# Kernel optimization log

Measured on AMD Instinct MI355X. Metric: run time of the kernel, lower is better.

Reference implementation:

```python
import jax, jax.numpy as jnp
import numpy as np

EMBED = 512
HEADS = 8
HEAD_DIM = EMBED // HEADS


def setup_inputs() -> dict:
    key = jax.random.key(0)
    ks = jax.random.split(key, 9)
    N, L = 4, 2048
    values = jax.random.normal(ks[0], (N, L, EMBED), dtype=jnp.float32)
    keys = jax.random.normal(ks[1], (N, L, EMBED), dtype=jnp.float32)
    query = jax.random.normal(ks[2], (N, L, EMBED), dtype=jnp.float32)
    mask = jax.random.randint(ks[3], (N, 1, 1, L), 0, 2, dtype=jnp.int32)
    s_h = 1.0 / np.sqrt(HEAD_DIM).astype(np.float32)
    s_e = 1.0 / np.sqrt(EMBED).astype(np.float32)
    Wv = jax.random.normal(ks[4], (HEAD_DIM, HEAD_DIM), dtype=jnp.float32) * s_h
    Wk = jax.random.normal(ks[5], (HEAD_DIM, HEAD_DIM), dtype=jnp.float32) * s_h
    Wq = jax.random.normal(ks[6], (HEAD_DIM, HEAD_DIM), dtype=jnp.float32) * s_h
    Wo = jax.random.normal(ks[7], (EMBED, EMBED), dtype=jnp.float32) * s_e
    bo = jnp.zeros((EMBED,), dtype=jnp.float32)
    return {"values": values, "keys": keys, "query": query, "mask": mask,
            "Wv": Wv, "Wk": Wk, "Wq": Wq, "Wo": Wo, "bo": bo}


def reference(values, keys, query, mask, Wv, Wk, Wq, Wo, bo):
    N, Lq, E = query.shape
    D = Wv.shape[0]
    H = E // D
    Lk = keys.shape[1]
    # split heads: [N, L, H, D]
    v = values.reshape(N, values.shape[1], H, D)
    k = keys.reshape(N, Lk, H, D)
    q = query.reshape(N, Lq, H, D)
    # per-head linear projections (nn.Linear: x @ W^T, no bias)
    v = jnp.einsum("nlhd,ed->nlhe", v, Wv)
    k = jnp.einsum("nlhd,ed->nlhe", k, Wk)
    q = jnp.einsum("nlhd,ed->nlhe", q, Wq)
    # energy: [N, H, Lq, Lk]
    energy = jnp.einsum("nqhd,nkhd->nhqk", q, k)
    energy = jnp.where(mask == 0, jnp.float32(-1e20), energy)
    # NOTE: original scales by sqrt(embed_size), not sqrt(head_dim)
    attn = jax.nn.softmax(energy / jnp.sqrt(jnp.float32(E)), axis=3)
    out = jnp.einsum("nhqk,nkhd->nqhd", attn, v).reshape(N, Lq, E)
    return out @ Wo.T + bo
```

## Files before the change

### kernel.cpp

```cpp
#include <hip/hip_runtime.h>

#define LSEQ 2048
#define EMB  512
#define NH   8
#define HD   64
#define NBATCH 4
#define QSCALE (0.044194173824159216f * 1.4426950408889634f)

using short8  = __attribute__((ext_vector_type(8))) short;
using short4v = __attribute__((ext_vector_type(4))) short;
using f32x4   = __attribute__((ext_vector_type(4))) float;

__device__ __forceinline__ short bf16r(float f) {
  union { float f; unsigned u; } x; x.f = f;
  unsigned r = x.u + 0x7FFFu + ((x.u >> 16) & 1u);
  return (short)(r >> 16);
}

__device__ __forceinline__ float exp2v(float x) {
  float r;
  asm("v_exp_f32 %0, %1" : "=v"(r) : "v"(x));
  return r;
}

__device__ __forceinline__ unsigned cvtpk(float lo, float hi) {
  unsigned r;
  asm("v_cvt_pk_bf16_f32 %0, %1, %2" : "=v"(r) : "v"(lo), "v"(hi));
  return r;
}

__device__ __forceinline__ void stage16(const void* g, void* l) {
  __builtin_amdgcn_global_load_lds(
      (const __attribute__((address_space(1))) unsigned int*)g,
      (__attribute__((address_space(3))) unsigned int*)l, 16, 0, 0);
}

__device__ __forceinline__ short8 cvt8(const float* __restrict__ p) {
  float4 a = ((const float4*)p)[0];
  float4 b = ((const float4*)p)[1];
  short8 r;
  r[0]=bf16r(a.x); r[1]=bf16r(a.y); r[2]=bf16r(a.z); r[3]=bf16r(a.w);
  r[4]=bf16r(b.x); r[5]=bf16r(b.y); r[6]=bf16r(b.z); r[7]=bf16r(b.w);
  return r;
}

__device__ __forceinline__ short8 ld8(const short* __restrict__ p) {
  return *(const short8*)p;
}

__global__ __launch_bounds__(256) void prep_kernel(
    const int* __restrict__ mask, float* __restrict__ fbias,
    int* __restrict__ kidx, int* __restrict__ meta,
    const float* __restrict__ Wq, const float* __restrict__ Wk,
    const float* __restrict__ Wv, short* __restrict__ Wqb,
    short* __restrict__ Wkb, short* __restrict__ Wvb) {
  __shared__ int ssum[256];
  int b = blockIdx.x;
  int tid = threadIdx.x;
  if (b < 4) {
    int n = b;
    int base = n * LSEQ;
    int loc[8], c = 0;
#pragma unroll
    for (int j = 0; j < 8; j++) { loc[j] = mask[base + tid * 8 + j] != 0; c += loc[j]; }
    ssum[tid] = c;
    __syncthreads();
    for (int off = 1; off < 256; off <<= 1) {
      int v = (tid >= off) ? ssum[tid - off] : 0;
      __syncthreads();
      ssum[tid] += v;
      __syncthreads();
    }
    int total = ssum[255];
    int excl = ssum[tid] - c;
    int qz = (total == 0);
#pragma unroll
    for (int j = 0; j < 8; j++) {
      int i = tid * 8 + j;
      kidx[base + i] = qz ? i : 0;
      fbias[base + i] = (qz || i < total) ? 0.f : -1e30f;
    }
    __syncthreads();
    if (!qz) {
      int pos = excl;
#pragma unroll
      for (int j = 0; j < 8; j++)
        if (loc[j]) { kidx[base + pos] = tid * 8 + j; pos++; }
    }
    if (tid == 0) {
      meta[n] = qz ? (LSEQ / 64) : ((total + 63) >> 6);
      meta[4 + n] = qz;
    }
  } else {
    int t = (b - 4) >> 2;
    int i = ((b - 4) & 3) * 256 + tid;
    const float* W = (t == 0) ? Wq : (t == 1) ? Wk : Wv;
    short* O = (t == 0) ? Wqb : (t == 1) ? Wkb : Wvb;
    float sc = (t == 0) ? QSCALE : 1.f;
    float4 v = ((const float4*)W)[i];
    short4v r;
    r[0]=bf16r(v.x*sc); r[1]=bf16r(v.y*sc); r[2]=bf16r(v.z*sc); r[3]=bf16r(v.w*sc);
    ((short4v*)O)[i] = r;
  }
}

__global__ __launch_bounds__(256) void proj_kernel(
    const float* __restrict__ keys, const float* __restrict__ values,
    const short* __restrict__ Wkb, const short* __restrict__ Wvb,
    const int* __restrict__ kidx, const int* __restrict__ meta,
    short* __restrict__ Kp, short* __restrict__ Vt) {
  __shared__ short tile[64][72];
  int t = blockIdx.y + 1;
  const float* x = (t == 1) ? keys : values;
  const short* W = (t == 1) ? Wkb  : Wvb;
  int idx = blockIdx.x;
  int lt = idx & 31, h = (idx >> 5) & 7, n = idx >> 8;
  int tid = threadIdx.x, lane = tid & 63, w = tid >> 6;
  int row16 = lane & 15, g = lane >> 4;
  int lbase = lt * 64 + w * 16;

  if (lbase >= ((meta[n] + 1) & ~1) * 64) return;
  int gidx = kidx[n * LSEQ + lbase + row16];
  const float* xr = x + ((size_t)(n * LSEQ + gidx)) * EMB + h * HD + g * 8;
  short8 a0 = cvt8(xr);
  short8 a1 = cvt8(xr + 32);

  f32x4 acc[4];
#pragma unroll
  for (int et = 0; et < 4; et++) acc[et] = (f32x4){0.f, 0.f, 0.f, 0.f};
#pragma unroll
  for (int et = 0; et < 4; et++) {
    const short* wr = W + (size_t)(et * 16 + row16) * HD + g * 8;
    short8 b0 = ld8(wr);
    short8 b1 = ld8(wr + 32);
    acc[et] = __builtin_amdgcn_mfma_f32_16x16x32_bf16(a0, b0, acc[et], 0, 0, 0);
    acc[et] = __builtin_amdgcn_mfma_f32_16x16x32_bf16(a1, b1, acc[et], 0, 0, 0);
  }

  if (t == 2) {
#pragma unroll
    for (int et = 0; et < 4; et++)
#pragma unroll
      for (int r = 0; r < 4; r++)
        tile[et * 16 + row16][w * 16 + g * 4 + r] = bf16r(acc[et][r]);
  } else {
#pragma unroll
    for (int et = 0; et < 4; et++)
#pragma unroll
      for (int r = 0; r < 4; r++)
        tile[w * 16 + g * 4 + r][et * 16 + row16] = bf16r(acc[et][r]);
  }
  __syncthreads();

  size_t nh = (size_t)(n * NH + h);
#pragma unroll
  for (int i = tid; i < 512; i += 256) {
    int rr = i >> 3, cc = i & 7;
    short8 v = *(const short8*)&tile[rr][cc * 8];
    if (t == 2)
      *(short8*)(Vt + (nh * HD + rr) * LSEQ + lt * 64 + cc * 8) = v;
    else
      *(short8*)(Kp + (nh * LSEQ + lt * 64 + rr) * HD + cc * 8) = v;
  }
}

__global__ __launch_bounds__(512, 1) void attn_kernel(
    const float* __restrict__ query, const short* __restrict__ Wqb,
    const short* __restrict__ Kp, const short* __restrict__ Vt,
    const float* __restrict__ fbias, const int* __restrict__ meta,
    short* __restrict__ aout, const float* __restrict__ Wo,
    short* __restrict__ Wob) {
  __shared__ __align__(16) char smem[98304];

  int idx = blockIdx.x;
  int tid = threadIdx.x;
  if (idx >= NBATCH * NH * (LSEQ / 256)) {
    int i = (idx - NBATCH * NH * (LSEQ / 256)) * 512 + tid;
    float4 v = ((const float4*)Wo)[i];
    short4v r;
    r[0]=bf16r(v.x); r[1]=bf16r(v.y); r[2]=bf16r(v.z); r[3]=bf16r(v.w);
    ((short4v*)Wob)[i] = r;
    return;
  }
  int h = idx & 7;
  int qt = (idx >> 3) & 7;
  int n = idx >> 6;
  int lane = tid & 63, w = tid >> 6;
  int q0 = lane & 15, g = lane >> 4;
  int xr = q0 & 7;
  int nkt = (meta[n] + 1) >> 1;

  size_t nh = (size_t)(n * NH + h);

  const char* Ksrc = (const char*)(Kp + nh * (size_t)LSEQ * HD);
  const char* Vsrc = (const char*)(Vt + nh * (size_t)HD * LSEQ);
  const float* fb  = fbias + n * LSEQ + g * 4;

  int ksoff[2], vsoff[2], ldo[2];
#pragma unroll
  for (int j = 0; j < 2; j++) {
    int c = j * 512 + w * 64 + lane;
    int rK = c >> 3, cwK = (c & 7) ^ (rK & 7);
    ksoff[j] = rK * 128 + cwK * 16;
    int rV = c >> 4, cwV = c & 15;
    int sub = (cwV & 7) ^ (rV & 7);
    vsoff[j] = rV * (LSEQ * 2) + ((cwV & 8) + sub) * 16;
    ldo[j] = (j * 512 + w * 64) * 16;
  }

  int kfragb = q0 * 128 + ((g ^ xr) << 4);
  int vfragb = q0 * 256 + ((g ^ xr) << 4);
  int pbase = 65536 + w * 4096 + q0 * 128;
  char* pw_[4];
#pragma unroll
  for (int ks = 0; ks < 4; ks++)
    pw_[ks] = smem + pbase + ((ks * 32 + g * 8) ^ (xr << 4));
  const char* pr0 = smem + pbase + ((g * 16) ^ (xr << 4));
  const char* pr1 = smem + pbase + ((64 + g * 16) ^ (xr << 4));

#pragma unroll
  for (int j = 0; j < 2; j++) stage16(Ksrc + ksoff[j], smem + ldo[j]);
#pragma unroll
  for (int j = 0; j < 2; j++) stage16(Vsrc + vsoff[j], smem + 32768 + ldo[j]);

  {
    short8 wf0[4], wf1[4];
#pragma unroll
    for (int et = 0; et < 4; et++) {
      wf0[et] = ld8(Wqb + (et * 16 + q0) * HD + g * 8);
      wf1[et] = ld8(Wqb + (et * 16 + q0) * HD + 32 + g * 8);
    }
    int zq = meta[4 + n];
#pragma unroll
    for (int hh = 0; hh < 2; hh++) {
      const float* xrow = query +
          ((size_t)(n * LSEQ + qt * 256 + w * 32 + hh * 16 + q0)) * EMB +
          h * HD + g * 8;
      short8 xa0 = cvt8(xrow);
      short8 xa1 = cvt8(xrow + 32);
#pragma unroll
      for (int et = 0; et < 4; et++) {
        f32x4 tq = (f32x4){0.f, 0.f, 0.f, 0.f};
        tq = __builtin_amdgcn_mfma_f32_16x16x32_bf16(wf0[et], xa0, tq, 0, 0, 0);
        tq = __builtin_amdgcn_mfma_f32_16x16x32_bf16(wf1[et], xa1, tq, 0, 0, 0);
        if (zq) tq = (f32x4){0.f, 0.f, 0.f, 0.f};
        *(int2*)(smem + pbase + hh * 2048 + ((et * 32 + g * 8) ^ (xr << 4))) =
            make_int2((int)cvtpk(tq[0], tq[1]), (int)cvtpk(tq[2], tq[3]));
      }
    }
  }
  asm volatile("s_waitcnt lgkmcnt(0)" ::: "memory");
  short8 bq00 = *(const short8*)pr0;
  short8 bq01 = *(const short8*)pr1;
  short8 bq10 = *(const short8*)(pr0 + 2048);
  short8 bq11 = *(const short8*)(pr1 + 2048);

  f32x4 acc0[4], acc1[4];
#pragma unroll
  for (int dt = 0; dt < 4; dt++) {
    acc0[dt] = (f32x4){0.f, 0.f, 0.f, 0.f};
    acc1[dt] = (f32x4){0.f, 0.f, 0.f, 0.f};
  }
  float l0 = 0.f, l1 = 0.f;

  __syncthreads();

  for (int kt = 0; kt < nkt; kt++) {
    int buf = kt & 1;
    if (kt < nkt - 1) {
      int bo = (buf ^ 1) * 16384;
      const char* Kn = Ksrc + (size_t)(kt + 1) * (128 * 128);
      const char* Vn = Vsrc + (size_t)(kt + 1) * 256;
#pragma unroll
      for (int j = 0; j < 2; j++) stage16(Kn + ksoff[j], smem + bo + ldo[j]);
#pragma unroll
      for (int j = 0; j < 2; j++) stage16(Vn + vsoff[j], smem + 32768 + bo + ldo[j]);
    }

#pragma unroll
    for (int h2 = 0; h2 < 2; h2++) {
      f32x4 fbv[4];
#pragma unroll
      for (int ks = 0; ks < 4; ks++)
        fbv[ks] = *(const f32x4*)(fb + kt * 128 + h2 * 64 + ks * 16);

      int kb_l = buf * 16384 + h2 * 8192 + kfragb;
      f32x4 s0[4], s1[4];
      __builtin_amdgcn_s_setprio(1);
#pragma unroll
      for (int ks = 0; ks < 4; ks++) {
        short8 k0 = *(const short8*)(smem + (kb_l + ks * 2048));
        short8 k1 = *(const short8*)(smem + ((kb_l + ks * 2048) ^ 64));
        f32x4 t0 = __builtin_amdgcn_mfma_f32_16x16x32_bf16(k0, bq00, fbv[ks], 0, 0, 0);
        s0[ks]   = __builtin_amdgcn_mfma_f32_16x16x32_bf16(k1, bq01, t0, 0, 0, 0);
        f32x4 t1 = __builtin_amdgcn_mfma_f32_16x16x32_bf16(k0, bq10, fbv[ks], 0, 0, 0);
        s1[ks]   = __builtin_amdgcn_mfma_f32_16x16x32_bf16(k1, bq11, t1, 0, 0, 0);
      }
      __builtin_amdgcn_s_setprio(0);

      float ps0 = 0.f, ps1 = 0.f;
#pragma unroll
      for (int ks = 0; ks < 4; ks++) {
        float p0 = exp2v(s0[ks][0] - 32.f), p1 = exp2v(s0[ks][1] - 32.f);
        float p2 = exp2v(s0[ks][2] - 32.f), p3 = exp2v(s0[ks][3] - 32.f);
        ps0 += (p0 + p1) + (p2 + p3);
        *(int2*)pw_[ks] = make_int2((int)cvtpk(p0, p1), (int)cvtpk(p2, p3));
        float q1 = exp2v(s1[ks][0] - 32.f), q2 = exp2v(s1[ks][1] - 32.f);
        float q3 = exp2v(s1[ks][2] - 32.f), q4 = exp2v(s1[ks][3] - 32.f);
        ps1 += (q1 + q2) + (q3 + q4);
        *(int2*)(pw_[ks] + 2048) = make_int2((int)cvtpk(q1, q2), (int)cvtpk(q3, q4));
      }
      l0 += ps0; l1 += ps1;

      asm volatile("s_waitcnt lgkmcnt(0)" ::: "memory");

      short8 ap00 = *(const short8*)pr0;
      short8 ap01 = *(const short8*)pr1;
      short8 ap10 = *(const short8*)(pr0 + 2048);
      short8 ap11 = *(const short8*)(pr1 + 2048);
      int vb_l = 32768 + buf * 16384 + vfragb + h2 * 128;
      __builtin_amdgcn_s_setprio(1);
#pragma unroll
      for (int dt = 0; dt < 4; dt++) {
        short8 v0 = *(const short8*)(smem + (vb_l + dt * 4096));
        short8 v1 = *(const short8*)(smem + ((vb_l + dt * 4096) ^ 64));
        acc0[dt] = __builtin_amdgcn_mfma_f32_16x16x32_bf16(ap00, v0, acc0[dt], 0, 0, 0);
        acc0[dt] = __builtin_amdgcn_mfma_f32_16x16x32_bf16(ap01, v1, acc0[dt], 0, 0, 0);
        acc1[dt] = __builtin_amdgcn_mfma_f32_16x16x32_bf16(ap10, v0, acc1[dt], 0, 0, 0);
        acc1[dt] = __builtin_amdgcn_mfma_f32_16x16x32_bf16(ap11, v1, acc1[dt], 0, 0, 0);
      }
      __builtin_amdgcn_s_setprio(0);
    }

    __syncthreads();
  }

  l0 += __shfl_xor(l0, 16);  l0 += __shfl_xor(l0, 32);
  l1 += __shfl_xor(l1, 16);  l1 += __shfl_xor(l1, 32);
  float li0 = l0 > 0.f ? 1.f / l0 : 0.f;
  float li1 = l1 > 0.f ? 1.f / l1 : 0.f;
  int lb = lane & 48;
  float w0[4], w1[4];
#pragma unroll
  for (int r = 0; r < 4; r++) {
    w0[r] = __shfl(li0, lb + g * 4 + r);
    w1[r] = __shfl(li1, lb + g * 4 + r);
  }
  int qrow = qt * 256 + w * 32;
#pragma unroll
  for (int r = 0; r < 4; r++) {
    size_t o0 = ((size_t)(n * LSEQ + qrow + g * 4 + r)) * EMB + h * HD;
    size_t o1 = ((size_t)(n * LSEQ + qrow + 16 + g * 4 + r)) * EMB + h * HD;
#pragma unroll
    for (int dt = 0; dt < 4; dt++) {
      aout[o0 + dt * 16 + q0] = bf16r(acc0[dt][r] * w0[r]);
      aout[o1 + dt * 16 + q0] = bf16r(acc1[dt][r] * w1[r]);
    }
  }
}

__global__ __launch_bounds__(256) void outproj_kernel(
    const short* __restrict__ aout, const short* __restrict__ Wob,
    const float* __restrict__ bo, float* __restrict__ out) {
  int mt = blockIdx.x, nt = blockIdx.y;
  int tid = threadIdx.x, lane = tid & 63, w = tid >> 6;
  int row16 = lane & 15, g = lane >> 4;
  int mrow = mt * 256 + w * 64;

  f32x4 acc[4][4];
#pragma unroll
  for (int hh = 0; hh < 4; hh++)
#pragma unroll
    for (int et = 0; et < 4; et++) acc[hh][et] = (f32x4){0.f, 0.f, 0.f, 0.f};

  for (int kc = 0; kc < 16; kc++) {
    short8 a[4];
#pragma unroll
    for (int hh = 0; hh < 4; hh++)
      a[hh] = ld8(aout + (size_t)(mrow + hh * 16 + row16) * EMB + kc * 32 + g * 8);
#pragma unroll
    for (int et = 0; et < 4; et++) {
      short8 bw = ld8(Wob + (size_t)(nt * 64 + et * 16 + row16) * EMB + kc * 32 + g * 8);
#pragma unroll
      for (int hh = 0; hh < 4; hh++)
        acc[hh][et] = __builtin_amdgcn_mfma_f32_16x16x32_bf16(a[hh], bw, acc[hh][et], 0, 0, 0);
    }
  }
#pragma unroll
  for (int et = 0; et < 4; et++) {
    int e = nt * 64 + et * 16 + row16;
    float bias = bo[e];
#pragma unroll
    for (int hh = 0; hh < 4; hh++)
#pragma unroll
      for (int r = 0; r < 4; r++)
        out[(size_t)(mrow + hh * 16 + g * 4 + r) * EMB + e] = acc[hh][et][r] + bias;
  }
}

extern "C" void kernel_launch(void* const* d_in, const int* in_sizes, int n_in,
                              void* d_out, int out_size, void* d_ws, size_t ws_size,
                              hipStream_t stream) {
  const float* values = (const float*)d_in[0];
  const float* keys   = (const float*)d_in[1];
  const float* query  = (const float*)d_in[2];
  const int*   mask   = (const int*)d_in[3];
  const float* Wv     = (const float*)d_in[4];
  const float* Wk     = (const float*)d_in[5];
  const float* Wq     = (const float*)d_in[6];
  const float* Wo     = (const float*)d_in[7];
  const float* bo     = (const float*)d_in[8];
  float* out = (float*)d_out;

  short* Kp = (short*)d_out;
  char* ws = (char*)d_ws;
  short* Vt    = (short*)(ws);
  short* aout  = (short*)(ws + (8u << 20));
  short* Wob   = (short*)(ws + (16u << 20));
  float* fbias = (float*)(ws + (16u << 20) + (512u << 10));
  int*   kidx  = (int*)  (ws + (16u << 20) + (544u << 10));
  int*   meta  = (int*)  (ws + (16u << 20) + (576u << 10));
  short* Wqb   = (short*)(ws + (16u << 20) + (577u << 10));
  short* Wkb   = (short*)(ws + (16u << 20) + (585u << 10));
  short* Wvb   = (short*)(ws + (16u << 20) + (593u << 10));

  prep_kernel<<<16, 256, 0, stream>>>(mask, fbias, kidx, meta,
                                      Wq, Wk, Wv, Wqb, Wkb, Wvb);
  proj_kernel<<<dim3(NBATCH * NH * (LSEQ / 64), 2), 256, 0, stream>>>(
      keys, values, Wkb, Wvb, kidx, meta, Kp, Vt);
  attn_kernel<<<NBATCH * NH * (LSEQ / 256) + 128, 512, 0, stream>>>(
      query, Wqb, Kp, Vt, fbias, meta, aout, Wo, Wob);
  outproj_kernel<<<dim3((NBATCH * LSEQ) / 256, EMB / 64), 256, 0, stream>>>(
      aout, Wob, bo, out);
}
```

Measured before the change: 78.77 us.

## Halve attention tile sizes to raise occupancy and double grid size

The attention kernel now handles 128 query rows per block (16 per wave) instead of 256, and uses 64-key tiles instead of 128. Shared memory drops to 48KB and launch bounds allow several blocks per CU, so the grid of 512 work blocks can fill more of the GPU with better latency hiding. In exchange each staged K/V tile is reused by fewer query rows and there are twice as many barrier-synchronised iterations. The loop count now comes directly from meta instead of being halved.

```diff
diff --git a/kernel.cpp b/kernel.cpp
--- a/kernel.cpp
+++ b/kernel.cpp
@@ -164,18 +164,18 @@
   }
 }
 
-__global__ __launch_bounds__(512, 1) void attn_kernel(
+__global__ __launch_bounds__(512, 4) void attn_kernel(
     const float* __restrict__ query, const short* __restrict__ Wqb,
     const short* __restrict__ Kp, const short* __restrict__ Vt,
     const float* __restrict__ fbias, const int* __restrict__ meta,
     short* __restrict__ aout, const float* __restrict__ Wo,
     short* __restrict__ Wob) {
-  __shared__ __align__(16) char smem[98304];
+  __shared__ __align__(16) char smem[49152];
 
   int idx = blockIdx.x;
   int tid = threadIdx.x;
-  if (idx >= NBATCH * NH * (LSEQ / 256)) {
-    int i = (idx - NBATCH * NH * (LSEQ / 256)) * 512 + tid;
+  if (idx >= NBATCH * NH * (LSEQ / 128)) {
+    int i = (idx - NBATCH * NH * (LSEQ / 128)) * 512 + tid;
     float4 v = ((const float4*)Wo)[i];
     short4v r;
     r[0]=bf16r(v.x); r[1]=bf16r(v.y); r[2]=bf16r(v.z); r[3]=bf16r(v.w);
@@ -183,12 +183,12 @@
     return;
   }
   int h = idx & 7;
-  int qt = (idx >> 3) & 7;
-  int n = idx >> 6;
+  int qt = (idx >> 3) & 15;
+  int n = idx >> 7;
   int lane = tid & 63, w = tid >> 6;
   int q0 = lane & 15, g = lane >> 4;
   int xr = q0 & 7;
-  int nkt = (meta[n] + 1) >> 1;
+  int nkt = meta[n];
 
   size_t nh = (size_t)(n * NH + h);
 
@@ -196,21 +196,14 @@
   const char* Vsrc = (const char*)(Vt + nh * (size_t)HD * LSEQ);
   const float* fb  = fbias + n * LSEQ + g * 4;
 
-  int ksoff[2], vsoff[2], ldo[2];
-#pragma unroll
-  for (int j = 0; j < 2; j++) {
-    int c = j * 512 + w * 64 + lane;
-    int rK = c >> 3, cwK = (c & 7) ^ (rK & 7);
-    ksoff[j] = rK * 128 + cwK * 16;
-    int rV = c >> 4, cwV = c & 15;
-    int sub = (cwV & 7) ^ (rV & 7);
-    vsoff[j] = rV * (LSEQ * 2) + ((cwV & 8) + sub) * 16;
-    ldo[j] = (j * 512 + w * 64) * 16;
-  }
+  int c = w * 64 + lane;
+  int rr_ = c >> 3, cw_ = (c & 7) ^ (rr_ & 7);
+  int ksoff = rr_ * 128 + cw_ * 16;
+  int vsoff = rr_ * (LSEQ * 2) + cw_ * 16;
+  int ldo = (w * 64) * 16;
 
   int kfragb = q0 * 128 + ((g ^ xr) << 4);
-  int vfragb = q0 * 256 + ((g ^ xr) << 4);
-  int pbase = 65536 + w * 4096 + q0 * 128;
+  int pbase = 32768 + w * 2048 + q0 * 128;
   char* pw_[4];
 #pragma unroll
   for (int ks = 0; ks < 4; ks++)
@@ -218,10 +211,8 @@
   const char* pr0 = smem + pbase + ((g * 16) ^ (xr << 4));
   const char* pr1 = smem + pbase + ((64 + g * 16) ^ (xr << 4));
 
-#pragma unroll
-  for (int j = 0; j < 2; j++) stage16(Ksrc + ksoff[j], smem + ldo[j]);
-#pragma unroll
-  for (int j = 0; j < 2; j++) stage16(Vsrc + vsoff[j], smem + 32768 + ldo[j]);
+  stage16(Ksrc + ksoff, smem + ldo);
+  stage16(Vsrc + vsoff, smem + 16384 + ldo);
 
   {
     short8 wf0[4], wf1[4];
@@ -231,131 +222,98 @@
       wf1[et] = ld8(Wqb + (et * 16 + q0) * HD + 32 + g * 8);
     }
     int zq = meta[4 + n];
-#pragma unroll
-    for (int hh = 0; hh < 2; hh++) {
-      const float* xrow = query +
-          ((size_t)(n * LSEQ + qt * 256 + w * 32 + hh * 16 + q0)) * EMB +
-          h * HD + g * 8;
-      short8 xa0 = cvt8(xrow);
-      short8 xa1 = cvt8(xrow + 32);
-#pragma unroll
-      for (int et = 0; et < 4; et++) {
-        f32x4 tq = (f32x4){0.f, 0.f, 0.f, 0.f};
-        tq = __builtin_amdgcn_mfma_f32_16x16x32_bf16(wf0[et], xa0, tq, 0, 0, 0);
-        tq = __builtin_amdgcn_mfma_f32_16x16x32_bf16(wf1[et], xa1, tq, 0, 0, 0);
-        if (zq) tq = (f32x4){0.f, 0.f, 0.f, 0.f};
-        *(int2*)(smem + pbase + hh * 2048 + ((et * 32 + g * 8) ^ (xr << 4))) =
-            make_int2((int)cvtpk(tq[0], tq[1]), (int)cvtpk(tq[2], tq[3]));
-      }
+    const float* xrow = query +
+        ((size_t)(n * LSEQ + qt * 128 + w * 16 + q0)) * EMB + h * HD + g * 8;
+    short8 xa0 = cvt8(xrow);
+    short8 xa1 = cvt8(xrow + 32);
+#pragma unroll
+    for (int et = 0; et < 4; et++) {
+      f32x4 tq = (f32x4){0.f, 0.f, 0.f, 0.f};
+      tq = __builtin_amdgcn_mfma_f32_16x16x32_bf16(wf0[et], xa0, tq, 0, 0, 0);
+      tq = __builtin_amdgcn_mfma_f32_16x16x32_bf16(wf1[et], xa1, tq, 0, 0, 0);
+      if (zq) tq = (f32x4){0.f, 0.f, 0.f, 0.f};
+      *(int2*)(smem + pbase + ((et * 32 + g * 8) ^ (xr << 4))) =
+          make_int2((int)cvtpk(tq[0], tq[1]), (int)cvtpk(tq[2], tq[3]));
     }
   }
   asm volatile("s_waitcnt lgkmcnt(0)" ::: "memory");
-  short8 bq00 = *(const short8*)pr0;
-  short8 bq01 = *(const short8*)pr1;
-  short8 bq10 = *(const short8*)(pr0 + 2048);
-  short8 bq11 = *(const short8*)(pr1 + 2048);
-
-  f32x4 acc0[4], acc1[4];
-#pragma unroll
-  for (int dt = 0; dt < 4; dt++) {
-    acc0[dt] = (f32x4){0.f, 0.f, 0.f, 0.f};
-    acc1[dt] = (f32x4){0.f, 0.f, 0.f, 0.f};
-  }
-  float l0 = 0.f, l1 = 0.f;
+  short8 bq0 = *(const short8*)pr0;
+  short8 bq1 = *(const short8*)pr1;
+
+  f32x4 acc[4];
+#pragma unroll
+  for (int dt = 0; dt < 4; dt++) acc[dt] = (f32x4){0.f, 0.f, 0.f, 0.f};
+  float lsum = 0.f;
 
   __syncthreads();
 
   for (int kt = 0; kt < nkt; kt++) {
     int buf = kt & 1;
     if (kt < nkt - 1) {
-      int bo = (buf ^ 1) * 16384;
-      const char* Kn = Ksrc + (size_t)(kt + 1) * (128 * 128);
-      const char* Vn = Vsrc + (size_t)(kt + 1) * 256;
-#pragma unroll
-      for (int j = 0; j < 2; j++) stage16(Kn + ksoff[j], smem + bo + ldo[j]);
-#pragma unroll
-      for (int j = 0; j < 2; j++) stage16(Vn + vsoff[j], smem + 32768 + bo + ldo[j]);
-    }
-
-#pragma unroll
-    for (int h2 = 0; h2 < 2; h2++) {
-      f32x4 fbv[4];
-#pragma unroll
-      for (int ks = 0; ks < 4; ks++)
-        fbv[ks] = *(const f32x4*)(fb + kt * 128 + h2 * 64 + ks * 16);
-
-      int kb_l = buf * 16384 + h2 * 8192 + kfragb;
-      f32x4 s0[4], s1[4];
-      __builtin_amdgcn_s_setprio(1);
-#pragma unroll
-      for (int ks = 0; ks < 4; ks++) {
-        short8 k0 = *(const short8*)(smem + (kb_l + ks * 2048));
-        short8 k1 = *(const short8*)(smem + ((kb_l + ks * 2048) ^ 64));
-        f32x4 t0 = __builtin_amdgcn_mfma_f32_16x16x32_bf16(k0, bq00, fbv[ks], 0, 0, 0);
-        s0[ks]   = __builtin_amdgcn_mfma_f32_16x16x32_bf16(k1, bq01, t0, 0, 0, 0);
-        f32x4 t1 = __builtin_amdgcn_mfma_f32_16x16x32_bf16(k0, bq10, fbv[ks], 0, 0, 0);
-        s1[ks]   = __builtin_amdgcn_mfma_f32_16x16x32_bf16(k1, bq11, t1, 0, 0, 0);
-      }
-      __builtin_amdgcn_s_setprio(0);
-
-      float ps0 = 0.f, ps1 = 0.f;
-#pragma unroll
-      for (int ks = 0; ks < 4; ks++) {
-        float p0 = exp2v(s0[ks][0] - 32.f), p1 = exp2v(s0[ks][1] - 32.f);
-        float p2 = exp2v(s0[ks][2] - 32.f), p3 = exp2v(s0[ks][3] - 32.f);
-        ps0 += (p0 + p1) + (p2 + p3);
-        *(int2*)pw_[ks] = make_int2((int)cvtpk(p0, p1), (int)cvtpk(p2, p3));
-        float q1 = exp2v(s1[ks][0] - 32.f), q2 = exp2v(s1[ks][1] - 32.f);
-        float q3 = exp2v(s1[ks][2] - 32.f), q4 = exp2v(s1[ks][3] - 32.f);
-        ps1 += (q1 + q2) + (q3 + q4);
-        *(int2*)(pw_[ks] + 2048) = make_int2((int)cvtpk(q1, q2), (int)cvtpk(q3, q4));
-      }
-      l0 += ps0; l1 += ps1;
-
-      asm volatile("s_waitcnt lgkmcnt(0)" ::: "memory");
-
-      short8 ap00 = *(const short8*)pr0;
-      short8 ap01 = *(const short8*)pr1;
-      short8 ap10 = *(const short8*)(pr0 + 2048);
-      short8 ap11 = *(const short8*)(pr1 + 2048);
-      int vb_l = 32768 + buf * 16384 + vfragb + h2 * 128;
-      __builtin_amdgcn_s_setprio(1);
-#pragma unroll
-      for (int dt = 0; dt < 4; dt++) {
-        short8 v0 = *(const short8*)(smem + (vb_l + dt * 4096));
-        short8 v1 = *(const short8*)(smem + ((vb_l + dt * 4096) ^ 64));
-        acc0[dt] = __builtin_amdgcn_mfma_f32_16x16x32_bf16(ap00, v0, acc0[dt], 0, 0, 0);
-        acc0[dt] = __builtin_amdgcn_mfma_f32_16x16x32_bf16(ap01, v1, acc0[dt], 0, 0, 0);
-        acc1[dt] = __builtin_amdgcn_mfma_f32_16x16x32_bf16(ap10, v0, acc1[dt], 0, 0, 0);
-        acc1[dt] = __builtin_amdgcn_mfma_f32_16x16x32_bf16(ap11, v1, acc1[dt], 0, 0, 0);
-      }
-      __builtin_amdgcn_s_setprio(0);
-    }
+      int bo = (buf ^ 1) * 8192;
+      stage16(Ksrc + (size_t)(kt + 1) * 8192 + ksoff, smem + bo + ldo);
+      stage16(Vsrc + (size_t)(kt + 1) * 128 + vsoff, smem + 16384 + bo + ldo);
+    }
+    f32x4 fbv[4];
+#pragma unroll
+    for (int ks = 0; ks < 4; ks++)
+      fbv[ks] = *(const f32x4*)(fb + kt * 64 + ks * 16);
+
+    int kb_l = buf * 8192 + kfragb;
+    f32x4 s[4];
+    __builtin_amdgcn_s_setprio(1);
+#pragma unroll
+    for (int ks = 0; ks < 4; ks++) {
+      short8 k0 = *(const short8*)(smem + (kb_l + ks * 2048));
+      short8 k1 = *(const short8*)(smem + ((kb_l + ks * 2048) ^ 64));
+      f32x4 t = __builtin_amdgcn_mfma_f32_16x16x32_bf16(k0, bq0, fbv[ks], 0, 0, 0);
+      s[ks]   = __builtin_amdgcn_mfma_f32_16x16x32_bf16(k1, bq1, t, 0, 0, 0);
+    }
+    __builtin_amdgcn_s_setprio(0);
+
+    float ps = 0.f;
+#pragma unroll
+    for (int ks = 0; ks < 4; ks++) {
+      float p0 = exp2v(s[ks][0] - 32.f), p1 = exp2v(s[ks][1] - 32.f);
+      float p2 = exp2v(s[ks][2] - 32.f), p3 = exp2v(s[ks][3] - 32.f);
+      ps += (p0 + p1) + (p2 + p3);
+      *(int2*)pw_[ks] = make_int2((int)cvtpk(p0, p1), (int)cvtpk(p2, p3));
+    }
+    lsum += ps;
+
+    asm volatile("s_waitcnt lgkmcnt(0)" ::: "memory");
+
+    short8 ap0 = *(const short8*)pr0;
+    short8 ap1 = *(const short8*)pr1;
+    int vb_l = 16384 + buf * 8192 + kfragb;
+    __builtin_amdgcn_s_setprio(1);
+#pragma unroll
+    for (int dt = 0; dt < 4; dt++) {
+      short8 v0 = *(const short8*)(smem + (vb_l + dt * 2048));
+      short8 v1 = *(const short8*)(smem + ((vb_l + dt * 2048) ^ 64));
+      acc[dt] = __builtin_amdgcn_mfma_f32_16x16x32_bf16(ap0, v0, acc[dt], 0, 0, 0);
+      acc[dt] = __builtin_amdgcn_mfma_f32_16x16x32_bf16(ap1, v1, acc[dt], 0, 0, 0);
+    }
+    __builtin_amdgcn_s_setprio(0);
 
     __syncthreads();
   }
 
-  l0 += __shfl_xor(l0, 16);  l0 += __shfl_xor(l0, 32);
-  l1 += __shfl_xor(l1, 16);  l1 += __shfl_xor(l1, 32);
-  float li0 = l0 > 0.f ? 1.f / l0 : 0.f;
-  float li1 = l1 > 0.f ? 1.f / l1 : 0.f;
+  lsum += __shfl_xor(lsum, 16);
+  lsum += __shfl_xor(lsum, 32);
+  float linv = lsum > 0.f ? 1.f / lsum : 0.f;
   int lb = lane & 48;
-  float w0[4], w1[4];
+  float li[4];
+#pragma unroll
+  for (int r = 0; r < 4; r++) li[r] = __shfl(linv, lb + g * 4 + r);
+
 #pragma unroll
   for (int r = 0; r < 4; r++) {
-    w0[r] = __shfl(li0, lb + g * 4 + r);
-    w1[r] = __shfl(li1, lb + g * 4 + r);
-  }
-  int qrow = qt * 256 + w * 32;
-#pragma unroll
-  for (int r = 0; r < 4; r++) {
-    size_t o0 = ((size_t)(n * LSEQ + qrow + g * 4 + r)) * EMB + h * HD;
-    size_t o1 = ((size_t)(n * LSEQ + qrow + 16 + g * 4 + r)) * EMB + h * HD;
-#pragma unroll
-    for (int dt = 0; dt < 4; dt++) {
-      aout[o0 + dt * 16 + q0] = bf16r(acc0[dt][r] * w0[r]);
-      aout[o1 + dt * 16 + q0] = bf16r(acc1[dt][r] * w1[r]);
-    }
+    int q = qt * 128 + w * 16 + g * 4 + r;
+#pragma unroll
+    for (int dt = 0; dt < 4; dt++)
+      aout[((size_t)(n * LSEQ + q)) * EMB + h * HD + dt * 16 + q0] =
+          bf16r(acc[dt][r] * li[r]);
   }
 }
 
@@ -428,7 +386,7 @@
                                       Wq, Wk, Wv, Wqb, Wkb, Wvb);
   proj_kernel<<<dim3(NBATCH * NH * (LSEQ / 64), 2), 256, 0, stream>>>(
       keys, values, Wkb, Wvb, kidx, meta, Kp, Vt);
-  attn_kernel<<<NBATCH * NH * (LSEQ / 256) + 128, 512, 0, stream>>>(
+  attn_kernel<<<NBATCH * NH * (LSEQ / 128) + 128, 512, 0, stream>>>(
       query, Wqb, Kp, Vt, fbias, meta, aout, Wo, Wob);
   outproj_kernel<<<dim3((NBATCH * LSEQ) / 256, EMB / 64), 256, 0, stream>>>(
       aout, Wob, bo, out);
```

Result: no change. 78.79 us (+0.0%).

## Triple-buffer K/V tiles with prefetch depth two and stage mask bias in LDS

Applied to the files above, without the earlier changes.

Replaces the double-buffered K/V staging with a three-slot ring buffer that prefetches two tiles ahead, using explicit vmcnt waits and raw s_barrier in place of __syncthreads. This lets each iteration wait only for the oldest outstanding loads, hiding more global-load latency. The per-key mask bias vector is also loaded once into shared memory instead of being read from global memory on every tile. Shared memory grows to 136 KB, which stays within a single block per CU, and correctness depends on the hand-counted vmcnt values matching the number of outstanding loads.

```diff
diff --git a/kernel.cpp b/kernel.cpp
--- a/kernel.cpp
+++ b/kernel.cpp
@@ -170,7 +170,7 @@
     const float* __restrict__ fbias, const int* __restrict__ meta,
     short* __restrict__ aout, const float* __restrict__ Wo,
     short* __restrict__ Wob) {
-  __shared__ __align__(16) char smem[98304];
+  __shared__ __align__(16) char smem[139264];
 
   int idx = blockIdx.x;
   int tid = threadIdx.x;
@@ -194,7 +194,6 @@
 
   const char* Ksrc = (const char*)(Kp + nh * (size_t)LSEQ * HD);
   const char* Vsrc = (const char*)(Vt + nh * (size_t)HD * LSEQ);
-  const float* fb  = fbias + n * LSEQ + g * 4;
 
   int ksoff[2], vsoff[2], ldo[2];
 #pragma unroll
@@ -210,7 +209,7 @@
 
   int kfragb = q0 * 128 + ((g ^ xr) << 4);
   int vfragb = q0 * 256 + ((g ^ xr) << 4);
-  int pbase = 65536 + w * 4096 + q0 * 128;
+  int pbase = 98304 + w * 4096 + q0 * 128;
   char* pw_[4];
 #pragma unroll
   for (int ks = 0; ks < 4; ks++)
@@ -218,10 +217,11 @@
   const char* pr0 = smem + pbase + ((g * 16) ^ (xr << 4));
   const char* pr1 = smem + pbase + ((64 + g * 16) ^ (xr << 4));
 
+  stage16(fbias + n * LSEQ + w * 256 + lane * 4, smem + 131072 + w * 1024);
 #pragma unroll
   for (int j = 0; j < 2; j++) stage16(Ksrc + ksoff[j], smem + ldo[j]);
 #pragma unroll
-  for (int j = 0; j < 2; j++) stage16(Vsrc + vsoff[j], smem + 32768 + ldo[j]);
+  for (int j = 0; j < 2; j++) stage16(Vsrc + vsoff[j], smem + 16384 + ldo[j]);
 
   {
     short8 wf0[4], wf1[4];
@@ -255,6 +255,13 @@
   short8 bq10 = *(const short8*)(pr0 + 2048);
   short8 bq11 = *(const short8*)(pr1 + 2048);
 
+  if (nkt > 1) {
+#pragma unroll
+    for (int j = 0; j < 2; j++) stage16(Ksrc + 16384 + ksoff[j], smem + 32768 + ldo[j]);
+#pragma unroll
+    for (int j = 0; j < 2; j++) stage16(Vsrc + 256 + vsoff[j], smem + 32768 + 16384 + ldo[j]);
+  }
+
   f32x4 acc0[4], acc1[4];
 #pragma unroll
   for (int dt = 0; dt < 4; dt++) {
@@ -263,18 +270,24 @@
   }
   float l0 = 0.f, l1 = 0.f;
 
-  __syncthreads();
-
+  if (nkt > 1)
+    asm volatile("s_waitcnt vmcnt(4)" ::: "memory");
+  else
+    asm volatile("s_waitcnt vmcnt(0)" ::: "memory");
+  __builtin_amdgcn_sched_barrier(0);
+  __builtin_amdgcn_s_barrier();
+
+  int cb = 0, sb = 2;
   for (int kt = 0; kt < nkt; kt++) {
-    int buf = kt & 1;
-    if (kt < nkt - 1) {
-      int bo = (buf ^ 1) * 16384;
-      const char* Kn = Ksrc + (size_t)(kt + 1) * (128 * 128);
-      const char* Vn = Vsrc + (size_t)(kt + 1) * 256;
-#pragma unroll
-      for (int j = 0; j < 2; j++) stage16(Kn + ksoff[j], smem + bo + ldo[j]);
-#pragma unroll
-      for (int j = 0; j < 2; j++) stage16(Vn + vsoff[j], smem + 32768 + bo + ldo[j]);
+    int bufo = cb * 32768;
+    if (kt + 2 < nkt) {
+      int sbo = sb * 32768;
+      const char* Kn = Ksrc + (size_t)(kt + 2) * 16384;
+      const char* Vn = Vsrc + (size_t)(kt + 2) * 256;
+#pragma unroll
+      for (int j = 0; j < 2; j++) stage16(Kn + ksoff[j], smem + sbo + ldo[j]);
+#pragma unroll
+      for (int j = 0; j < 2; j++) stage16(Vn + vsoff[j], smem + sbo + 16384 + ldo[j]);
     }
 
 #pragma unroll
@@ -282,9 +295,10 @@
       f32x4 fbv[4];
 #pragma unroll
       for (int ks = 0; ks < 4; ks++)
-        fbv[ks] = *(const f32x4*)(fb + kt * 128 + h2 * 64 + ks * 16);
-
-      int kb_l = buf * 16384 + h2 * 8192 + kfragb;
+        fbv[ks] = *(const f32x4*)(smem + 131072 +
+                                  (kt * 128 + h2 * 64 + ks * 16 + g * 4) * 4);
+
+      int kb_l = bufo + h2 * 8192 + kfragb;
       f32x4 s0[4], s1[4];
       __builtin_amdgcn_s_setprio(1);
 #pragma unroll
@@ -318,7 +332,7 @@
       short8 ap01 = *(const short8*)pr1;
       short8 ap10 = *(const short8*)(pr0 + 2048);
       short8 ap11 = *(const short8*)(pr1 + 2048);
-      int vb_l = 32768 + buf * 16384 + vfragb + h2 * 128;
+      int vb_l = bufo + 16384 + vfragb + h2 * 128;
       __builtin_amdgcn_s_setprio(1);
 #pragma unroll
       for (int dt = 0; dt < 4; dt++) {
@@ -332,7 +346,15 @@
       __builtin_amdgcn_s_setprio(0);
     }
 
-    __syncthreads();
+    if (kt + 2 < nkt)
+      asm volatile("s_waitcnt vmcnt(4)" ::: "memory");
+    else
+      asm volatile("s_waitcnt vmcnt(0)" ::: "memory");
+    __builtin_amdgcn_sched_barrier(0);
+    __builtin_amdgcn_s_barrier();
+
+    cb = (cb == 2) ? 0 : cb + 1;
+    sb = (sb == 2) ? 0 : sb + 1;
   }
 
   l0 += __shfl_xor(l0, 16);  l0 += __shfl_xor(l0, 32);
```

Measured after the change: 75.27 us, median of 2. -4.4%, faster.
